# Kernel tuning notes

Measured on AMD Instinct MI355X. Metric: run time of the kernel, lower is better.

Reference implementation:

```python
import jax, jax.numpy as jnp
import numpy as np

B, S, D, H = 4, 2048, 1024, 16
DK = D // H

def setup_inputs() -> dict:
    key = jax.random.key(0)
    ks = jax.random.split(key, 5)
    x = jax.random.normal(ks[0], (B, S, D), dtype=jnp.float32)
    scale = 1.0 / np.sqrt(D)
    Wq = jax.random.normal(ks[1], (D, D), dtype=jnp.float32) * scale
    Wk = jax.random.normal(ks[2], (D, D), dtype=jnp.float32) * scale
    Wv = jax.random.normal(ks[3], (D, D), dtype=jnp.float32) * scale
    Wo = jax.random.normal(ks[4], (D, D), dtype=jnp.float32) * scale
    return {"x": x, "Wq": Wq, "Wk": Wk, "Wv": Wv, "Wo": Wo}

def reference(x, Wq, Wk, Wv, Wo):
    # F.linear: y = x @ W.T  (weights stored torch-style [out, in])
    q = jnp.einsum('bsd,ed->bse', x, Wq).reshape(B, S, H, DK).transpose(0, 2, 1, 3)
    k = jnp.einsum('bsd,ed->bse', x, Wk).reshape(B, S, H, DK).transpose(0, 2, 1, 3)
    v = jnp.einsum('bsd,ed->bse', x, Wv).reshape(B, S, H, DK).transpose(0, 2, 1, 3)
    scores = jnp.einsum('bhqd,bhkd->bhqk', q, k) / jnp.sqrt(jnp.float32(DK))
    attn = jax.nn.softmax(scores, axis=-1)  # dropout p=0.0 -> identity
    out = jnp.einsum('bhqk,bhkd->bhqd', attn, v)
    out = out.transpose(0, 2, 1, 3).reshape(B, S, D)
    return jnp.einsum('bsd,ed->bse', out, Wo)
```

## Files before the change

### kernel.cpp

```cpp
#include <hip/hip_runtime.h>
#include <hip/hip_bf16.h>

#define B_ 4
#define S_ 2048
#define D_ 1024
#define H_ 16
#define DK_ 64

typedef __attribute__((ext_vector_type(8))) short short8;
typedef __attribute__((ext_vector_type(4))) float floatx4;
typedef __attribute__((ext_vector_type(16))) float floatx16;
typedef __attribute__((ext_vector_type(4))) unsigned int uint4v;

static __device__ __forceinline__ unsigned short f2bf(float f) {
    unsigned int u = __float_as_uint(f);
    u += 0x7fffu + ((u >> 16) & 1u);
    return (unsigned short)(u >> 16);
}

static __device__ __forceinline__ unsigned int pack2bf_fast(float a, float b) {
    unsigned int ua = (__float_as_uint(a) + 0x8000u) >> 16;
    unsigned int ub = (__float_as_uint(b) + 0x8000u) & 0xffff0000u;
    return ua | ub;
}

static __device__ __forceinline__ unsigned int pack2bf(float a, float b) {
    return (unsigned int)f2bf(a) | ((unsigned int)f2bf(b) << 16);
}

#define PLSWAP(a, b) asm volatile("v_permlane32_swap_b32 %0, %1" : "+v"(a), "+v"(b))

struct CastAll {
    const float* x;
    const float* w[4];
    unsigned short* xd;
    unsigned short* wd[4];
};

__global__ void cast_all_kernel(CastAll a) {
    int i = blockIdx.x * blockDim.x + threadIdx.x;
    const float* s;
    unsigned short* d;
    int j;
    if (i < 2097152) {
        s = a.x; d = a.xd; j = i;
    } else {
        int k = i - 2097152;
        int w = k >> 18;
        j = k & 262143;
        s = a.w[w]; d = a.wd[w];
    }
    float4 v = ((const float4*)s)[j];
    ushort4 o;
    o.x = f2bf(v.x); o.y = f2bf(v.y); o.z = f2bf(v.z); o.w = f2bf(v.w);
    ((ushort4*)d)[j] = o;
}

template <typename OutT, bool VT2>
__global__ __launch_bounds__(256) void gemm_bt(
    const unsigned short* __restrict__ A,
    const unsigned short* __restrict__ W0,
    const unsigned short* __restrict__ W1,
    const unsigned short* __restrict__ W2,
    OutT* __restrict__ C0, OutT* __restrict__ C1, OutT* __restrict__ C2,
    int M, int N, int K)
{
    __shared__ __align__(16) unsigned short At[128 * 64];
    __shared__ __align__(16) unsigned short Bt[128 * 64];

    const unsigned short* W = (blockIdx.z == 0) ? W0 : ((blockIdx.z == 1) ? W1 : W2);
    OutT* C = (blockIdx.z == 0) ? C0 : ((blockIdx.z == 1) ? C1 : C2);

    const int n0 = blockIdx.x * 128;
    const int m0 = blockIdx.y * 128;
    const int wv = threadIdx.x >> 6;
    const int ln = threadIdx.x & 63;
    const int quad = ln >> 4;
    const int l15 = ln & 15;
    const int wm = (wv >> 1) * 64;
    const int wn = (wv & 1) * 64;

    floatx4 acc[4][4];
#pragma unroll
    for (int i = 0; i < 4; i++)
#pragma unroll
        for (int j = 0; j < 4; j++) acc[i][j] = floatx4{0.f, 0.f, 0.f, 0.f};

    const int lr = ln >> 3;
    const int lc = (ln & 7) * 8;

    for (int k0 = 0; k0 < K; k0 += 64) {
        __syncthreads();
#pragma unroll
        for (int c = 0; c < 4; c++) {
            int rowA = wv * 32 + c * 8;
            const unsigned short* gA = A + (size_t)(m0 + rowA + lr) * K + k0 + lc;
            __builtin_amdgcn_global_load_lds(
                (const __attribute__((address_space(1))) void*)gA,
                (__attribute__((address_space(3))) void*)&At[rowA * 64], 16, 0, 0);
            const unsigned short* gB = W + (size_t)(n0 + rowA + lr) * K + k0 + lc;
            __builtin_amdgcn_global_load_lds(
                (const __attribute__((address_space(1))) void*)gB,
                (__attribute__((address_space(3))) void*)&Bt[rowA * 64], 16, 0, 0);
        }
        __syncthreads();

#pragma unroll
        for (int kk = 0; kk < 2; kk++) {
            short8 af[4], bf[4];
#pragma unroll
            for (int i = 0; i < 4; i++)
                af[i] = *(const short8*)&At[(wm + i * 16 + l15) * 64 + kk * 32 + quad * 8];
#pragma unroll
            for (int j = 0; j < 4; j++)
                bf[j] = *(const short8*)&Bt[(wn + j * 16 + l15) * 64 + kk * 32 + quad * 8];
#pragma unroll
            for (int i = 0; i < 4; i++)
#pragma unroll
                for (int j = 0; j < 4; j++)
                    acc[i][j] = __builtin_amdgcn_mfma_f32_16x16x32_bf16(af[i], bf[j], acc[i][j], 0, 0, 0);
        }
    }

    if constexpr (VT2) {
        if (blockIdx.z == 2) {
            unsigned short* Vt = (unsigned short*)C;
#pragma unroll
            for (int i = 0; i < 4; i++)
#pragma unroll
                for (int j = 0; j < 4; j++) {
                    int col = n0 + wn + j * 16 + l15;
                    int row0 = m0 + wm + i * 16 + quad * 4;
                    int bb = row0 >> 11, ss = row0 & 2047;
                    size_t addr = ((size_t)(bb * 1024 + col)) * 2048 + ss;
                    uint2 pk;
                    pk.x = pack2bf(acc[i][j][0], acc[i][j][1]);
                    pk.y = pack2bf(acc[i][j][2], acc[i][j][3]);
                    *(uint2*)((unsigned short*)Vt + addr) = pk;
                }
            return;
        }
    }

#pragma unroll
    for (int i = 0; i < 4; i++)
#pragma unroll
        for (int j = 0; j < 4; j++)
#pragma unroll
            for (int r = 0; r < 4; r++) {
                int row = m0 + wm + i * 16 + quad * 4 + r;
                int col = n0 + wn + j * 16 + l15;
                float v = acc[i][j][r];
                if constexpr (sizeof(OutT) == 2)
                    C[(size_t)row * N + col] = (OutT)f2bf(v);
                else
                    C[(size_t)row * N + col] = v;
            }
}

__global__ __launch_bounds__(256, 4) void flash_attn(
    const unsigned short* __restrict__ Q,
    const unsigned short* __restrict__ K,
    const unsigned short* __restrict__ Vt,
    unsigned short* __restrict__ O)
{
    __shared__ __align__(16) unsigned short Kt[64 * 72];
    __shared__ __align__(16) unsigned short VT[64 * 72];

    const int qt = blockIdx.x;
    const int h = blockIdx.y;
    const int b = blockIdx.z;
    const int tid = threadIdx.x;
    const int wv = tid >> 6;
    const int ln = tid & 63;
    const int l31 = ln & 31;
    const int half = ln >> 5;

    const size_t base = ((size_t)b * S_) * D_ + (size_t)h * DK_;
    const size_t vtbase = ((size_t)(b * 1024 + h * 64)) * (size_t)S_;

    const int qrow = qt * 128 + wv * 32 + l31;
    short8 qf[4];
    {
        const unsigned short* qp = Q + base + (size_t)qrow * D_ + half * 8;
#pragma unroll
        for (int ks = 0; ks < 4; ks++) qf[ks] = *(const short8*)(qp + ks * 16);
    }

    floatx16 Oacc[2];
#pragma unroll
    for (int mt = 0; mt < 2; mt++)
#pragma unroll
        for (int e = 0; e < 16; e++) Oacc[mt][e] = 0.f;
    float l_i = 0.f;

    const int srow = tid >> 3;
    const int scol = (tid & 7) * 8;

    const float scl = 1.4426950408889634f / 8.0f;
    const float CL = 12.0f;

    for (int kt = 0; kt < S_ / 64; kt++) {
        __syncthreads();
#pragma unroll
        for (int c = 0; c < 2; c++) {
            int row = srow + c * 32;
            *(short8*)&Kt[row * 72 + scol] =
                *(const short8*)(K + base + (size_t)(kt * 64 + row) * D_ + scol);
            *(short8*)&VT[row * 72 + scol] =
                *(const short8*)(Vt + vtbase + (size_t)row * S_ + kt * 64 + scol);
        }
        __syncthreads();

        floatx16 sac[2];
#pragma unroll
        for (int mt = 0; mt < 2; mt++) {
#pragma unroll
            for (int e = 0; e < 16; e++) sac[mt][e] = 0.f;
#pragma unroll
            for (int ks = 0; ks < 4; ks++) {
                short8 kf = *(const short8*)&Kt[(mt * 32 + l31) * 72 + ks * 16 + half * 8];
                sac[mt] = __builtin_amdgcn_mfma_f32_32x32x16_bf16(kf, qf[ks], sac[mt], 0, 0, 0);
            }
        }

        uint2 run[2][4];
#pragma unroll
        for (int mt = 0; mt < 2; mt++)
#pragma unroll
            for (int g = 0; g < 4; g++) {
                float p0 = __builtin_amdgcn_exp2f(fmaf(sac[mt][4 * g + 0], scl, -CL));
                float p1 = __builtin_amdgcn_exp2f(fmaf(sac[mt][4 * g + 1], scl, -CL));
                float p2 = __builtin_amdgcn_exp2f(fmaf(sac[mt][4 * g + 2], scl, -CL));
                float p3 = __builtin_amdgcn_exp2f(fmaf(sac[mt][4 * g + 3], scl, -CL));
                l_i += (p0 + p1) + (p2 + p3);
                run[mt][g].x = pack2bf_fast(p0, p1);
                run[mt][g].y = pack2bf_fast(p2, p3);
            }

#pragma unroll
        for (int mt = 0; mt < 2; mt++)
#pragma unroll
            for (int t = 0; t < 2; t++) {
                PLSWAP(run[mt][2 * t].x, run[mt][2 * t + 1].x);
                PLSWAP(run[mt][2 * t].y, run[mt][2 * t + 1].y);
            }

#pragma unroll
        for (int mt2 = 0; mt2 < 2; mt2++)
#pragma unroll
            for (int t = 0; t < 2; t++) {
                int ks = mt2 * 2 + t;
                uint4v u = {run[mt2][2 * t].x, run[mt2][2 * t].y,
                            run[mt2][2 * t + 1].x, run[mt2][2 * t + 1].y};
                short8 pf = __builtin_bit_cast(short8, u);
#pragma unroll
                for (int mt = 0; mt < 2; mt++) {
                    short8 vf = *(const short8*)&VT[(mt * 32 + l31) * 72 + ks * 16 + half * 8];
                    Oacc[mt] = __builtin_amdgcn_mfma_f32_32x32x16_bf16(vf, pf, Oacc[mt], 0, 0, 0);
                }
            }
    }

    l_i += __shfl_xor(l_i, 32);
    float inv = 1.0f / l_i;

#pragma unroll
    for (int mt = 0; mt < 2; mt++)
#pragma unroll
        for (int g = 0; g < 4; g++) {
            uint2 pk;
            pk.x = pack2bf(Oacc[mt][4 * g + 0] * inv, Oacc[mt][4 * g + 1] * inv);
            pk.y = pack2bf(Oacc[mt][4 * g + 2] * inv, Oacc[mt][4 * g + 3] * inv);
            *(uint2*)(O + base + (size_t)qrow * D_ + mt * 32 + 8 * g + 4 * half) = pk;
        }
}

extern "C" void kernel_launch(void* const* d_in, const int* in_sizes, int n_in,
                              void* d_out, int out_size, void* d_ws, size_t ws_size,
                              hipStream_t stream) {
    const float* x  = (const float*)d_in[0];
    const float* Wq = (const float*)d_in[1];
    const float* Wk = (const float*)d_in[2];
    const float* Wv = (const float*)d_in[3];
    const float* Wo = (const float*)d_in[4];
    float* out = (float*)d_out;

    char* ws = (char*)d_ws;
    const size_t MB = 1024 * 1024;
    unsigned short* xb  = (unsigned short*)(ws);
    unsigned short* wqb = (unsigned short*)(ws + 16 * MB);
    unsigned short* wkb = (unsigned short*)(ws + 18 * MB);
    unsigned short* wvb = (unsigned short*)(ws + 20 * MB);
    unsigned short* wob = (unsigned short*)(ws + 22 * MB);
    unsigned short* Qb  = (unsigned short*)(ws + 24 * MB);
    unsigned short* Kb  = (unsigned short*)(ws + 40 * MB);
    unsigned short* Vtb = (unsigned short*)(ws + 56 * MB);
    unsigned short* Ob  = (unsigned short*)(ws);

    CastAll ca;
    ca.x = x; ca.xd = xb;
    ca.w[0] = Wq; ca.w[1] = Wk; ca.w[2] = Wv; ca.w[3] = Wo;
    ca.wd[0] = wqb; ca.wd[1] = wkb; ca.wd[2] = wvb; ca.wd[3] = wob;
    cast_all_kernel<<<12288, 256, 0, stream>>>(ca);

    dim3 gq(D_ / 128, (B_ * S_) / 128, 3);
    gemm_bt<unsigned short, true><<<gq, 256, 0, stream>>>(
        xb, wqb, wkb, wvb, Qb, Kb, Vtb, B_ * S_, D_, D_);

    dim3 gf(S_ / 128, H_, B_);
    flash_attn<<<gf, 256, 0, stream>>>(Qb, Kb, Vtb, Ob);

    dim3 go(D_ / 128, (B_ * S_) / 128, 1);
    gemm_bt<float, false><<<go, 256, 0, stream>>>(
        Ob, wob, wob, wob, out, out, out, B_ * S_, D_, D_);
}
```

Before: 310.1 us.

## Fold softmax scale into Q projection, compute row sums via MFMA, use 32x32 GEMM tiles

The Q projection epilogue now multiplies by log2(e)/sqrt(dk), so attention can call exp2 directly on the scores without a per-element FMA. The -12 clamp offset is dropped, which raises the risk of overflow or precision issues with no running max. The softmax denominator is now accumulated with an extra MFMA against a ones vector instead of scalar adds plus a cross-lane shuffle. The bf16 pack uses v_perm, and the projection GEMM switches from 16x16x32 to 32x32x16 MFMA tiles.

After: 341.4 us. +10.1%, slower.

```diff
diff --git a/kernel.cpp b/kernel.cpp
--- a/kernel.cpp
+++ b/kernel.cpp
@@ -12,16 +12,18 @@
 typedef __attribute__((ext_vector_type(16))) float floatx16;
 typedef __attribute__((ext_vector_type(4))) unsigned int uint4v;
 
+#define QSCL 0.1803368801111204f
+
 static __device__ __forceinline__ unsigned short f2bf(float f) {
     unsigned int u = __float_as_uint(f);
     u += 0x7fffu + ((u >> 16) & 1u);
     return (unsigned short)(u >> 16);
 }
 
-static __device__ __forceinline__ unsigned int pack2bf_fast(float a, float b) {
-    unsigned int ua = (__float_as_uint(a) + 0x8000u) >> 16;
-    unsigned int ub = (__float_as_uint(b) + 0x8000u) & 0xffff0000u;
-    return ua | ub;
+static __device__ __forceinline__ unsigned int pack2bf_perm(float a, float b) {
+    unsigned int u0 = __float_as_uint(a) + 0x8000u;
+    unsigned int u1 = __float_as_uint(b) + 0x8000u;
+    return __builtin_amdgcn_perm(u1, u0, 0x07060302u);
 }
 
 static __device__ __forceinline__ unsigned int pack2bf(float a, float b) {
@@ -75,16 +77,18 @@
     const int m0 = blockIdx.y * 128;
     const int wv = threadIdx.x >> 6;
     const int ln = threadIdx.x & 63;
-    const int quad = ln >> 4;
-    const int l15 = ln & 15;
+    const int l31 = ln & 31;
+    const int half = ln >> 5;
     const int wm = (wv >> 1) * 64;
     const int wn = (wv & 1) * 64;
 
-    floatx4 acc[4][4];
-#pragma unroll
-    for (int i = 0; i < 4; i++)
-#pragma unroll
-        for (int j = 0; j < 4; j++) acc[i][j] = floatx4{0.f, 0.f, 0.f, 0.f};
+    floatx16 acc[2][2];
+#pragma unroll
+    for (int mt = 0; mt < 2; mt++)
+#pragma unroll
+        for (int nt = 0; nt < 2; nt++)
+#pragma unroll
+            for (int e = 0; e < 16; e++) acc[mt][nt][e] = 0.f;
 
     const int lr = ln >> 3;
     const int lc = (ln & 7) * 8;
@@ -106,56 +110,62 @@
         __syncthreads();
 
 #pragma unroll
-        for (int kk = 0; kk < 2; kk++) {
-            short8 af[4], bf[4];
-#pragma unroll
-            for (int i = 0; i < 4; i++)
-                af[i] = *(const short8*)&At[(wm + i * 16 + l15) * 64 + kk * 32 + quad * 8];
-#pragma unroll
-            for (int j = 0; j < 4; j++)
-                bf[j] = *(const short8*)&Bt[(wn + j * 16 + l15) * 64 + kk * 32 + quad * 8];
-#pragma unroll
-            for (int i = 0; i < 4; i++)
-#pragma unroll
-                for (int j = 0; j < 4; j++)
-                    acc[i][j] = __builtin_amdgcn_mfma_f32_16x16x32_bf16(af[i], bf[j], acc[i][j], 0, 0, 0);
-        }
-    }
+        for (int ks = 0; ks < 4; ks++) {
+            short8 af[2], bf[2];
+#pragma unroll
+            for (int mt = 0; mt < 2; mt++)
+                af[mt] = *(const short8*)&At[(wm + mt * 32 + l31) * 64 + ks * 16 + half * 8];
+#pragma unroll
+            for (int nt = 0; nt < 2; nt++)
+                bf[nt] = *(const short8*)&Bt[(wn + nt * 32 + l31) * 64 + ks * 16 + half * 8];
+#pragma unroll
+            for (int mt = 0; mt < 2; mt++)
+#pragma unroll
+                for (int nt = 0; nt < 2; nt++)
+                    acc[mt][nt] = __builtin_amdgcn_mfma_f32_32x32x16_bf16(af[mt], bf[nt], acc[mt][nt], 0, 0, 0);
+        }
+    }
+
+    const float esc = (VT2 && blockIdx.z == 0) ? QSCL : 1.0f;
 
     if constexpr (VT2) {
         if (blockIdx.z == 2) {
             unsigned short* Vt = (unsigned short*)C;
 #pragma unroll
-            for (int i = 0; i < 4; i++)
-#pragma unroll
-                for (int j = 0; j < 4; j++) {
-                    int col = n0 + wn + j * 16 + l15;
-                    int row0 = m0 + wm + i * 16 + quad * 4;
-                    int bb = row0 >> 11, ss = row0 & 2047;
-                    size_t addr = ((size_t)(bb * 1024 + col)) * 2048 + ss;
-                    uint2 pk;
-                    pk.x = pack2bf(acc[i][j][0], acc[i][j][1]);
-                    pk.y = pack2bf(acc[i][j][2], acc[i][j][3]);
-                    *(uint2*)((unsigned short*)Vt + addr) = pk;
+            for (int mt = 0; mt < 2; mt++)
+#pragma unroll
+                for (int nt = 0; nt < 2; nt++)
+#pragma unroll
+                    for (int rg = 0; rg < 4; rg++) {
+                        int col = n0 + wn + nt * 32 + l31;
+                        int row0 = m0 + wm + mt * 32 + 4 * half + 8 * rg;
+                        int bb = row0 >> 11, ss = row0 & 2047;
+                        size_t addr = ((size_t)(bb * 1024 + col)) * 2048 + ss;
+                        uint2 pk;
+                        pk.x = pack2bf(acc[mt][nt][4 * rg + 0], acc[mt][nt][4 * rg + 1]);
+                        pk.y = pack2bf(acc[mt][nt][4 * rg + 2], acc[mt][nt][4 * rg + 3]);
+                        *(uint2*)(Vt + addr) = pk;
+                    }
+            return;
+        }
+    }
+
+#pragma unroll
+    for (int mt = 0; mt < 2; mt++)
+#pragma unroll
+        for (int nt = 0; nt < 2; nt++)
+#pragma unroll
+            for (int rg = 0; rg < 4; rg++)
+#pragma unroll
+                for (int r = 0; r < 4; r++) {
+                    int row = m0 + wm + mt * 32 + 4 * half + 8 * rg + r;
+                    int col = n0 + wn + nt * 32 + l31;
+                    float v = acc[mt][nt][4 * rg + r] * esc;
+                    if constexpr (sizeof(OutT) == 2)
+                        C[(size_t)row * N + col] = (OutT)f2bf(v);
+                    else
+                        C[(size_t)row * N + col] = v;
                 }
-            return;
-        }
-    }
-
-#pragma unroll
-    for (int i = 0; i < 4; i++)
-#pragma unroll
-        for (int j = 0; j < 4; j++)
-#pragma unroll
-            for (int r = 0; r < 4; r++) {
-                int row = m0 + wm + i * 16 + quad * 4 + r;
-                int col = n0 + wn + j * 16 + l15;
-                float v = acc[i][j][r];
-                if constexpr (sizeof(OutT) == 2)
-                    C[(size_t)row * N + col] = (OutT)f2bf(v);
-                else
-                    C[(size_t)row * N + col] = v;
-            }
 }
 
 __global__ __launch_bounds__(256, 4) void flash_attn(
@@ -187,18 +197,20 @@
         for (int ks = 0; ks < 4; ks++) qf[ks] = *(const short8*)(qp + ks * 16);
     }
 
-    floatx16 Oacc[2];
+    short8 ones;
+#pragma unroll
+    for (int e = 0; e < 8; e++) ones[e] = (short)0x3F80;
+
+    floatx16 Oacc[2], lacc;
 #pragma unroll
     for (int mt = 0; mt < 2; mt++)
 #pragma unroll
         for (int e = 0; e < 16; e++) Oacc[mt][e] = 0.f;
-    float l_i = 0.f;
+#pragma unroll
+    for (int e = 0; e < 16; e++) lacc[e] = 0.f;
 
     const int srow = tid >> 3;
     const int scol = (tid & 7) * 8;
-
-    const float scl = 1.4426950408889634f / 8.0f;
-    const float CL = 12.0f;
 
     for (int kt = 0; kt < S_ / 64; kt++) {
         __syncthreads();
@@ -229,13 +241,12 @@
         for (int mt = 0; mt < 2; mt++)
 #pragma unroll
             for (int g = 0; g < 4; g++) {
-                float p0 = __builtin_amdgcn_exp2f(fmaf(sac[mt][4 * g + 0], scl, -CL));
-                float p1 = __builtin_amdgcn_exp2f(fmaf(sac[mt][4 * g + 1], scl, -CL));
-                float p2 = __builtin_amdgcn_exp2f(fmaf(sac[mt][4 * g + 2], scl, -CL));
-                float p3 = __builtin_amdgcn_exp2f(fmaf(sac[mt][4 * g + 3], scl, -CL));
-                l_i += (p0 + p1) + (p2 + p3);
-                run[mt][g].x = pack2bf_fast(p0, p1);
-                run[mt][g].y = pack2bf_fast(p2, p3);
+                float p0 = __builtin_amdgcn_exp2f(sac[mt][4 * g + 0]);
+                float p1 = __builtin_amdgcn_exp2f(sac[mt][4 * g + 1]);
+                float p2 = __builtin_amdgcn_exp2f(sac[mt][4 * g + 2]);
+                float p3 = __builtin_amdgcn_exp2f(sac[mt][4 * g + 3]);
+                run[mt][g].x = pack2bf_perm(p0, p1);
+                run[mt][g].y = pack2bf_perm(p2, p3);
             }
 
 #pragma unroll
@@ -259,11 +270,11 @@
                     short8 vf = *(const short8*)&VT[(mt * 32 + l31) * 72 + ks * 16 + half * 8];
                     Oacc[mt] = __builtin_amdgcn_mfma_f32_32x32x16_bf16(vf, pf, Oacc[mt], 0, 0, 0);
                 }
+                lacc = __builtin_amdgcn_mfma_f32_32x32x16_bf16(ones, pf, lacc, 0, 0, 0);
             }
     }
 
-    l_i += __shfl_xor(l_i, 32);
-    float inv = 1.0f / l_i;
+    float inv = 1.0f / lacc[0];
 
 #pragma unroll
     for (int mt = 0; mt < 2; mt++)
```
